# Performance work log

Hardware: AMD Instinct MI355X
Metric: run time of the kernel (lower is better)

## Reference

```python
import jax, jax.numpy as jnp
import numpy as np
import math

B, S, D, H, HD = 2, 2048, 2048, 16, 128
ROPE_THETA = 10000.0


def _rope_cache(seq_len, dim, base, dtype=jnp.float32):
    inv_freq = 1.0 / (base ** (jnp.arange(0, dim, 2, dtype=jnp.float32) / dim))
    t = jnp.arange(seq_len, dtype=jnp.float32)
    freqs = jnp.einsum('i,j->ij', t, inv_freq)          # [S, dim/2]
    emb = jnp.concatenate([freqs, freqs], axis=-1)       # [S, dim]
    return jnp.cos(emb).astype(dtype), jnp.sin(emb).astype(dtype)


def _rotate_half(x):
    x1, x2 = x[..., : x.shape[-1] // 2], x[..., x.shape[-1] // 2:]
    return jnp.concatenate([-x2, x1], axis=-1)


def setup_inputs() -> dict:
    key = jax.random.key(0)
    ks = jax.random.split(key, 6)
    hidden_states = jax.random.normal(ks[0], (B, S, D), dtype=jnp.float32) * 0.02
    w_scale = 1.0 / math.sqrt(D)
    Wq = jax.random.normal(ks[1], (D, D), dtype=jnp.float32) * w_scale
    Wk = jax.random.normal(ks[2], (D, D), dtype=jnp.float32) * w_scale
    Wv = jax.random.normal(ks[3], (D, D), dtype=jnp.float32) * w_scale
    Wo = jax.random.normal(ks[4], (D, D), dtype=jnp.float32) * w_scale
    # additive causal mask [B, 1, S, S]: 0 on/below diag, large negative above
    causal = jnp.tril(jnp.ones((S, S), dtype=bool))
    attention_mask = jnp.where(causal, 0.0, -1e9).astype(jnp.float32)
    attention_mask = jnp.broadcast_to(attention_mask[None, None], (B, 1, S, S))
    position_ids = jnp.broadcast_to(jnp.arange(S, dtype=jnp.int32)[None], (B, S))
    return {
        'hidden_states': hidden_states,
        'attention_mask': attention_mask,
        'position_ids': position_ids,
        'Wq': Wq, 'Wk': Wk, 'Wv': Wv, 'Wo': Wo,
    }


def reference(hidden_states, attention_mask, position_ids, Wq, Wk, Wv, Wo):
    bsz, q_len, _ = hidden_states.shape
    # projections (torch Linear: x @ W.T), then split heads -> [B, H, S, HD]
    def proj(W):
        return jnp.einsum('bsd,ed->bse', hidden_states, W).reshape(bsz, q_len, H, HD).transpose(0, 2, 1, 3)
    q, k, v = proj(Wq), proj(Wk), proj(Wv)
    cos_c, sin_c = _rope_cache(q_len, HD, ROPE_THETA, hidden_states.dtype)
    cos = cos_c[position_ids][:, None]  # [B, 1, S, HD]
    sin = sin_c[position_ids][:, None]
    q = q * cos + _rotate_half(q) * sin
    k = k * cos + _rotate_half(k) * sin
    scores = jnp.einsum('bhqd,bhkd->bhqk', q, k) / math.sqrt(HD)
    scores = scores + attention_mask
    attn_weights = jax.nn.softmax(scores.astype(jnp.float32), axis=-1).astype(q.dtype)
    attn_out = jnp.einsum('bhqk,bhkd->bhqd', attn_weights, v)
    attn_out = attn_out.transpose(0, 2, 1, 3).reshape(bsz, q_len, D)
    out = jnp.einsum('bsd,ed->bse', attn_out, Wo)
    return out
```

## Files before the change

kernel.cpp:

```cpp
#include <hip/hip_runtime.h>

typedef __bf16 bf16;
typedef __bf16 bf16x8 __attribute__((ext_vector_type(8)));
typedef float f32x4 __attribute__((ext_vector_type(4)));

#define D_MODEL 2048
#define SEQ 2048
#define NH 16
#define HEAD_DIM 128
#define NBATCH 2
#define SM_SCALE 0.08838834764831845f
#define WSEG 4194304
#define NT_TILES 32

typedef __attribute__((address_space(1))) const void* gas_cp;
typedef __attribute__((address_space(3))) void* las_p;
__device__ __forceinline__ void ll16(const bf16* g, bf16* l) {
  __builtin_amdgcn_global_load_lds((gas_cp)g, (las_p)l, 16, 0, 0);
}

__device__ __forceinline__ bf16x8 cvt8(const float* p) {
  float4 a = *(const float4*)p;
  float4 b = *(const float4*)(p + 4);
  bf16x8 v;
  v[0] = (bf16)a.x; v[1] = (bf16)a.y; v[2] = (bf16)a.z; v[3] = (bf16)a.w;
  v[4] = (bf16)b.x; v[5] = (bf16)b.y; v[6] = (bf16)b.z; v[7] = (bf16)b.w;
  return v;
}

__global__ __launch_bounds__(256)
void cvt_hidden(const float* __restrict__ src, bf16* __restrict__ dst) {
  size_t i = ((size_t)blockIdx.x * 256 + threadIdx.x) * 8;
  *(bf16x8*)(dst + i) = cvt8(src + i);
}

__global__ __launch_bounds__(256)
void cvt_weights(const float* __restrict__ w0, const float* __restrict__ w1,
                 const float* __restrict__ w2, const float* __restrict__ w3,
                 bf16* __restrict__ dst) {
  const float* src = (blockIdx.y == 0) ? w0 : (blockIdx.y == 1) ? w1
                   : (blockIdx.y == 2) ? w2 : w3;
  size_t i = ((size_t)blockIdx.x * 256 + threadIdx.x) * 8;
  *(bf16x8*)(dst + (size_t)blockIdx.y * WSEG + i) = cvt8(src + i);
}

#define LDFRAG(DA, DB, SB, KX)                                               \
  _Pragma("unroll") for (int mi = 0; mi < 4; mi++)                           \
      DA[mi] = *(const bf16x8*)((SB) + ((arow + mi * 16) << 7) + (KX));      \
  DB[0] = *(const bf16x8*)((SB) + 16384 + (rb0 << 7) + (KX));                \
  DB[1] = *(const bf16x8*)((SB) + 16384 + (rb1 << 7) + (KX));                \
  DB[2] = *(const bf16x8*)((SB) + 16384 + (rb2 << 7) + (KX));                \
  DB[3] = *(const bf16x8*)((SB) + 16384 + (rb3 << 7) + (KX));

#define MMAC(AF, BF)                                                         \
  _Pragma("unroll") for (int mi = 0; mi < 4; mi++)                           \
  _Pragma("unroll") for (int ni = 0; ni < 4; ni++)                           \
      acc[mi][ni] = __builtin_amdgcn_mfma_f32_16x16x32_bf16(                 \
          AF[mi], BF[ni], acc[mi][ni], 0, 0, 0);

#define ST1(GP, ROW0, KT, LB)                                                \
  ll16((GP) + (size_t)((ROW0) + w * 8 + l8) * D_MODEL + (KT) * 64 + kelem,   \
       (bf16*)((LB) + w * 1024));

template <typename TC, int MODE, int NBN>
__global__ __launch_bounds__(512, 2)
void gemm128(const bf16* __restrict__ A, const bf16* __restrict__ W,
             TC* __restrict__ C, bf16* __restrict__ Qo, bf16* __restrict__ Ko,
             bf16* __restrict__ Vo, const int* __restrict__ pos_ids) {
  __shared__ __align__(16) char smem[147456];

  const int tid  = threadIdx.x;
  const int lane = tid & 63;
  const int w    = tid >> 6;
  const int quad = lane >> 4, l15 = lane & 15;
  const int l8   = lane >> 3, l7 = lane & 7;
  const int kelem = 8 * (l7 ^ l8);
  const int wm = w >> 2;
  const int wn = w & 3;
  const int hh = wn >> 1;
  const int cb = (wn & 1) * 32;

  const int nwg = 32 * NBN;
  const int bid = blockIdx.x;
  const int lin = (bid & 7) * (nwg >> 3) + (bid >> 3);
  const int by = lin / NBN, bx = lin % NBN;
  const int mBase = by << 7, nBase = bx << 8;

  const int kx0 = (quad * 16) ^ ((l15 & 7) << 4);
  const int kx1 = kx0 ^ 64;
  const int arow = wm * 64 + l15;
  const int rb0 = hh * 128 + cb + l15;
  const int rb1 = rb0 + 16, rb2 = rb0 + 64, rb3 = rb0 + 80;

  f32x4 acc[4][4];
#pragma unroll
  for (int i = 0; i < 4; i++)
#pragma unroll
    for (int j = 0; j < 4; j++) acc[i][j] = 0.0f;

  bf16x8 aP[4], bP[4];
  bf16x8 aQ[4], bQ[4];

  {
    char* s0 = smem;
    char* s1 = smem + 49152;
    ST1(A, mBase,       0, s0 + 0);
    ST1(A, mBase + 64,  0, s0 + 8192);
    ST1(W, nBase,       0, s0 + 16384);
    ST1(W, nBase + 64,  0, s0 + 24576);
    ST1(W, nBase + 128, 0, s0 + 32768);
    ST1(W, nBase + 192, 0, s0 + 40960);
    ST1(A, mBase,       1, s1 + 0);
    ST1(A, mBase + 64,  1, s1 + 8192);
    ST1(W, nBase,       1, s1 + 16384);
    ST1(W, nBase + 64,  1, s1 + 24576);
    ST1(W, nBase + 128, 1, s1 + 32768);
    ST1(W, nBase + 192, 1, s1 + 40960);
  }
  asm volatile("s_waitcnt vmcnt(6)" ::: "memory");
  __builtin_amdgcn_s_barrier();
  LDFRAG(aP, bP, smem, kx0);

  int buf = 0;
  for (int t = 0; t < NT_TILES; ++t) {
    char* const Sb  = smem + buf * 49152;
    const int  nb1  = (buf + 1 == 3) ? 0 : buf + 1;
    const int  pb   = (buf + 2 >= 3) ? buf - 1 : buf + 2;
    char* const Nb  = smem + nb1 * 49152;
    char* const Pb  = smem + pb * 49152;
    const bool pf   = (t + 2 < NT_TILES);

    LDFRAG(aQ, bQ, Sb, kx1);
    if (pf) {
      ST1(A, mBase,      t + 2, Pb + 0);
      ST1(A, mBase + 64, t + 2, Pb + 8192);
      ST1(W, nBase,      t + 2, Pb + 16384);
    }
    __builtin_amdgcn_sched_barrier(0);
    __builtin_amdgcn_s_setprio(1);
    MMAC(aP, bP);
    __builtin_amdgcn_s_setprio(0);
    asm volatile("s_waitcnt lgkmcnt(0)" ::: "memory");
    if (pf)
      asm volatile("s_waitcnt vmcnt(3)" ::: "memory");
    else
      asm volatile("s_waitcnt vmcnt(0)" ::: "memory");
    __builtin_amdgcn_s_barrier();

    if (t + 1 < NT_TILES) {
      LDFRAG(aP, bP, Nb, kx0);
    }
    if (pf) {
      ST1(W, nBase + 64,  t + 2, Pb + 24576);
      ST1(W, nBase + 128, t + 2, Pb + 32768);
      ST1(W, nBase + 192, t + 2, Pb + 40960);
    }
    __builtin_amdgcn_sched_barrier(0);
    __builtin_amdgcn_s_setprio(1);
    MMAC(aQ, bQ);
    __builtin_amdgcn_s_setprio(0);
    asm volatile("s_waitcnt lgkmcnt(0)" ::: "memory");
    __builtin_amdgcn_s_barrier();

    buf = nb1;
  }

  if (MODE == 0) {
#pragma unroll
    for (int mi = 0; mi < 4; mi++) {
      const int m = mBase + wm * 64 + mi * 16 + quad * 4;
#pragma unroll
      for (int ni = 0; ni < 4; ni++) {
        const int n = nBase + hh * 128 + cb + (ni & 1) * 16 + (ni >> 1) * 64 + l15;
        TC* cp = C + (size_t)m * D_MODEL + n;
#pragma unroll
        for (int r = 0; r < 4; r++) cp[(size_t)r * D_MODEL] = (TC)acc[mi][ni][r];
      }
    }
  } else {
    const int matrix = nBase >> 11;
    const int nb     = nBase & 2047;
    if (matrix == 2) {
      const int h = (nb >> 7) + hh;
#pragma unroll
      for (int mi = 0; mi < 4; mi++)
#pragma unroll
        for (int ni = 0; ni < 4; ni++) {
          const int hd = cb + (ni & 1) * 16 + (ni >> 1) * 64 + l15;
#pragma unroll
          for (int r = 0; r < 4; r++) {
            int m = mBase + wm * 64 + mi * 16 + quad * 4 + r;
            int b = m >> 11, s2 = m & 2047;
            Vo[((size_t)((b * NH + h) * HEAD_DIM + hd)) * SEQ + s2] =
                (bf16)acc[mi][ni][r];
          }
        }
    } else {
      bf16* Out = (matrix == 0) ? Qo : Ko;
      float invf[2];
#pragma unroll
      for (int ni = 0; ni < 2; ni++)
        invf[ni] = __expf(-(float)(cb + ni * 16 + l15) *
                          (9.210340371976184f / 64.0f));
#pragma unroll
      for (int mi = 0; mi < 4; mi++)
#pragma unroll
        for (int r = 0; r < 4; r++) {
          int m = mBase + wm * 64 + mi * 16 + quad * 4 + r;
          float pos = (float)pos_ids[m];
          bf16* op = Out + (size_t)m * D_MODEL + nb + hh * 128 + cb + l15;
#pragma unroll
          for (int ni = 0; ni < 2; ni++) {
            float sn, cs;
            __sincosf(pos * invf[ni], &sn, &cs);
            float q0 = acc[mi][ni][r];
            float q1 = acc[mi][ni + 2][r];
            op[ni * 16]      = (bf16)(q0 * cs - q1 * sn);
            op[ni * 16 + 64] = (bf16)(q1 * cs + q0 * sn);
          }
        }
    }
  }
}

__global__ __launch_bounds__(256, 3)
void attn_mfma(const bf16* __restrict__ Q, const bf16* __restrict__ K,
               const bf16* __restrict__ Vt, bf16* __restrict__ O) {
  __shared__ __align__(16) bf16 K_lds[64 * 136];
  __shared__ __align__(16) bf16 V_lds[128 * 72];
  __shared__ __align__(16) bf16 P_lds[64 * 72];

  const int tid  = threadIdx.x;
  const int lane = tid & 63;
  const int w    = tid >> 6;
  const int quad = lane >> 4, l15 = lane & 15;
  const int s    = 31 - blockIdx.y;
  const int bh   = blockIdx.x;
  const size_t qkBase = (size_t)(bh >> 4) * SEQ * D_MODEL + (size_t)(bh & 15) * HEAD_DIM;
  const size_t vBase  = (size_t)bh * HEAD_DIM * SEQ;

  const int qbase = s * 64 + w * 16;

  bf16x8 qa[4];
#pragma unroll
  for (int kk = 0; kk < 4; kk++)
    qa[kk] = *(const bf16x8*)(Q + qkBase + (size_t)(qbase + l15) * D_MODEL + kk * 32 + quad * 8);

  bf16x8 ones;
#pragma unroll
  for (int i = 0; i < 8; i++) ones[i] = (bf16)1.0f;

  f32x4 oacc[8], ls;
#pragma unroll
  for (int ni = 0; ni < 8; ni++) oacc[ni] = 0.0f;
  ls = 0.0f;

  const int ntiles = s + 1;

  bf16x8 kr[4], vr[4];
  auto loadKV = [&](int t0) {
#pragma unroll
    for (int i = 0; i < 4; i++) {
      int c = tid + 256 * i;
      kr[i] = *(const bf16x8*)(K + qkBase + (size_t)(t0 + (c >> 4)) * D_MODEL + (c & 15) * 8);
    }
#pragma unroll
    for (int i = 0; i < 4; i++) {
      int c = tid + 256 * i;
      vr[i] = *(const bf16x8*)(Vt + vBase + (size_t)(c >> 3) * SEQ + t0 + (c & 7) * 8);
    }
  };
  loadKV(0);

  const int prow = w * 16;

  for (int tt = 0; tt < ntiles; tt++) {
    const int t0 = tt * 64;
    __syncthreads();
#pragma unroll
    for (int i = 0; i < 4; i++) {
      int c = tid + 256 * i;
      *(bf16x8*)&K_lds[(c >> 4) * 136 + (c & 15) * 8] = kr[i];
    }
#pragma unroll
    for (int i = 0; i < 4; i++) {
      int c = tid + 256 * i;
      *(bf16x8*)&V_lds[(c >> 3) * 72 + (c & 7) * 8] = vr[i];
    }
    __syncthreads();
    if (tt + 1 < ntiles) loadKV(t0 + 64);

    f32x4 sacc[4];
#pragma unroll
    for (int ni = 0; ni < 4; ni++) sacc[ni] = 0.0f;
#pragma unroll
    for (int kk = 0; kk < 4; kk++) {
#pragma unroll
      for (int ni = 0; ni < 4; ni++) {
        bf16x8 kf = *(const bf16x8*)&K_lds[(ni * 16 + l15) * 136 + kk * 32 + quad * 8];
        sacc[ni] = __builtin_amdgcn_mfma_f32_16x16x32_bf16(qa[kk], kf, sacc[ni], 0, 0, 0);
      }
    }

    if (tt == s) {
#pragma unroll
      for (int r = 0; r < 4; r++) {
        int qrow = qbase + quad * 4 + r;
#pragma unroll
        for (int ni = 0; ni < 4; ni++) {
          int tcol = t0 + ni * 16 + l15;
          float pv = (tcol <= qrow) ? __expf(fminf(sacc[ni][r] * SM_SCALE, 30.0f)) : 0.0f;
          P_lds[(prow + quad * 4 + r) * 72 + ni * 16 + l15] = (bf16)pv;
        }
      }
    } else {
#pragma unroll
      for (int r = 0; r < 4; r++)
#pragma unroll
        for (int ni = 0; ni < 4; ni++)
          P_lds[(prow + quad * 4 + r) * 72 + ni * 16 + l15] =
              (bf16)__expf(fminf(sacc[ni][r] * SM_SCALE, 30.0f));
    }

#pragma unroll
    for (int kk2 = 0; kk2 < 2; kk2++) {
      bf16x8 pf = *(const bf16x8*)&P_lds[(prow + l15) * 72 + kk2 * 32 + quad * 8];
#pragma unroll
      for (int ni = 0; ni < 8; ni++) {
        bf16x8 vf = *(const bf16x8*)&V_lds[(ni * 16 + l15) * 72 + kk2 * 32 + quad * 8];
        oacc[ni] = __builtin_amdgcn_mfma_f32_16x16x32_bf16(pf, vf, oacc[ni], 0, 0, 0);
      }
      ls = __builtin_amdgcn_mfma_f32_16x16x32_bf16(pf, ones, ls, 0, 0, 0);
    }
  }

#pragma unroll
  for (int r = 0; r < 4; r++) {
    float inv = 1.0f / ls[r];
    bf16* op = O + qkBase + (size_t)(qbase + quad * 4 + r) * D_MODEL;
#pragma unroll
    for (int ni = 0; ni < 8; ni++)
      op[ni * 16 + l15] = (bf16)(oacc[ni][r] * inv);
  }
}

extern "C" void kernel_launch(void* const* d_in, const int* in_sizes, int n_in,
                              void* d_out, int out_size, void* d_ws, size_t ws_size,
                              hipStream_t stream) {
  const float* hidden = (const float*)d_in[0];
  const int* pos = (const int*)d_in[2];
  const float* Wq = (const float*)d_in[3];
  const float* Wk = (const float*)d_in[4];
  const float* Wv = (const float*)d_in[5];
  const float* Wo = (const float*)d_in[6];
  float* out = (float*)d_out;

  const size_t TENS = (size_t)NBATCH * SEQ * D_MODEL;
  bf16* Qb = (bf16*)d_ws;
  bf16* Kb = Qb + TENS;
  bf16* Vt = Kb + TENS;
  bf16* AO = Vt + TENS;
  bf16* Hb = AO + TENS;
  bf16* Wb = Hb + TENS;

  cvt_hidden<<<dim3(TENS / 2048), dim3(256), 0, stream>>>(hidden, Hb);
  cvt_weights<<<dim3(WSEG / 2048, 4), dim3(256), 0, stream>>>(Wq, Wk, Wv, Wo, Wb);

  gemm128<bf16, 1, 24><<<dim3(768), dim3(512), 0, stream>>>(
      Hb, Wb, (bf16*)nullptr, Qb, Kb, Vt, pos);

  attn_mfma<<<dim3(NBATCH * NH, 32), dim3(256), 0, stream>>>(Qb, Kb, Vt, AO);

  gemm128<float, 0, 8><<<dim3(256), dim3(512), 0, stream>>>(
      AO, Wb + 3 * (size_t)WSEG, out, nullptr, nullptr, nullptr, nullptr);
}
```

Measured before the change: 364.6 us.

## Use 256x256 tile GEMM for QKV projection; specialize output projection kernel

Adds a new QKV projection kernel with 256x256 output tiles (8 waves, each computing 128x64). It uses a simpler double-buffered pipeline and keeps the fused RoPE and V-transpose epilogue. This halves the grid to 384 workgroups and raises arithmetic intensity per LDS load, aiming to cut global and LDS traffic per FLOP. The output projection becomes a non-templated kernel with a plainer column mapping. The larger tile doubles accumulator registers, which risks register pressure or spills under launch_bounds(512,2), and the new pipeline waits on vmcnt(0) every tile, giving less overlap.

New measurement: 370.4 us. Within noise of the previous version (+1.6%).

```diff
diff --git a/kernel.cpp b/kernel.cpp
--- a/kernel.cpp
+++ b/kernel.cpp
@@ -44,6 +44,157 @@
   *(bf16x8*)(dst + (size_t)blockIdx.y * WSEG + i) = cvt8(src + i);
 }
 
+#define LDF256(DA, DB, SB, KX)                                               \
+  _Pragma("unroll") for (int mi = 0; mi < 8; mi++)                           \
+      DA[mi] = *(const bf16x8*)((SB) + ((arowQ + mi * 16) << 7) + (KX));     \
+  DB[0] = *(const bf16x8*)((SB) + 32768 + (qb0 << 7) + (KX));                \
+  DB[1] = *(const bf16x8*)((SB) + 32768 + (qb1 << 7) + (KX));                \
+  DB[2] = *(const bf16x8*)((SB) + 32768 + (qb2 << 7) + (KX));                \
+  DB[3] = *(const bf16x8*)((SB) + 32768 + (qb3 << 7) + (KX));
+
+#define MM256(AF, BF)                                                        \
+  _Pragma("unroll") for (int mi = 0; mi < 8; mi++)                           \
+  _Pragma("unroll") for (int ni = 0; ni < 4; ni++)                           \
+      acc[mi][ni] = __builtin_amdgcn_mfma_f32_16x16x32_bf16(                 \
+          AF[mi], BF[ni], acc[mi][ni], 0, 0, 0);
+
+#define ST2(GP, ROW0, KT, LB)                                                \
+  ll16((GP) + (size_t)((ROW0) + w * 8 + l8) * D_MODEL + (KT) * 64 + kelem,   \
+       (bf16*)((LB) + w * 1024));
+
+__global__ __launch_bounds__(512, 2)
+void gemm256(const bf16* __restrict__ A, const bf16* __restrict__ W,
+             bf16* __restrict__ Qo, bf16* __restrict__ Ko,
+             bf16* __restrict__ Vo, const int* __restrict__ pos_ids) {
+  __shared__ __align__(16) char smem[131072];
+
+  const int tid  = threadIdx.x;
+  const int lane = tid & 63;
+  const int w    = tid >> 6;
+  const int quad = lane >> 4, l15 = lane & 15;
+  const int l8   = lane >> 3, l7 = lane & 7;
+  const int kelem = 8 * (l7 ^ l8);
+  const int wm2 = w >> 2;
+  const int wn2 = w & 3;
+  const int hh  = wn2 >> 1;
+  const int cb  = (wn2 & 1) * 32;
+
+  const int bid = blockIdx.x;
+  const int lin = (bid & 7) * 48 + (bid >> 3);
+  const int by = lin / 24, bx = lin % 24;
+  const int mBase = by << 8, nBase = bx << 8;
+
+  const int kx0 = (quad * 16) ^ ((l15 & 7) << 4);
+  const int kx1 = kx0 ^ 64;
+  const int arowQ = wm2 * 128 + l15;
+  const int qb0 = hh * 128 + cb + l15;
+  const int qb1 = qb0 + 16, qb2 = qb0 + 64, qb3 = qb0 + 80;
+
+  f32x4 acc[8][4];
+#pragma unroll
+  for (int i = 0; i < 8; i++)
+#pragma unroll
+    for (int j = 0; j < 4; j++) acc[i][j] = 0.0f;
+
+  bf16x8 aP[8], bP[4];
+  bf16x8 aQ[8], bQ[4];
+
+  {
+    char* s0 = smem;
+    ST2(A, mBase,       0, s0 + 0);
+    ST2(A, mBase + 64,  0, s0 + 8192);
+    ST2(A, mBase + 128, 0, s0 + 16384);
+    ST2(A, mBase + 192, 0, s0 + 24576);
+    ST2(W, nBase,       0, s0 + 32768);
+    ST2(W, nBase + 64,  0, s0 + 40960);
+    ST2(W, nBase + 128, 0, s0 + 49152);
+    ST2(W, nBase + 192, 0, s0 + 57344);
+  }
+  asm volatile("s_waitcnt vmcnt(0)" ::: "memory");
+  __builtin_amdgcn_s_barrier();
+  LDF256(aP, bP, smem, kx0);
+
+  int buf = 0;
+  for (int t = 0; t < NT_TILES; ++t) {
+    char* const Sb = smem + buf * 65536;
+    char* const Ob = smem + (buf ^ 1) * 65536;
+    const bool pf  = (t + 1 < NT_TILES);
+
+    LDF256(aQ, bQ, Sb, kx1);
+    if (pf) {
+      ST2(A, mBase,       t + 1, Ob + 0);
+      ST2(A, mBase + 64,  t + 1, Ob + 8192);
+      ST2(A, mBase + 128, t + 1, Ob + 16384);
+      ST2(A, mBase + 192, t + 1, Ob + 24576);
+      ST2(W, nBase,       t + 1, Ob + 32768);
+      ST2(W, nBase + 64,  t + 1, Ob + 40960);
+      ST2(W, nBase + 128, t + 1, Ob + 49152);
+      ST2(W, nBase + 192, t + 1, Ob + 57344);
+    }
+    __builtin_amdgcn_sched_barrier(0);
+    __builtin_amdgcn_s_setprio(1);
+    MM256(aP, bP);
+    __builtin_amdgcn_s_setprio(0);
+    asm volatile("s_waitcnt lgkmcnt(0)" ::: "memory");
+    asm volatile("s_waitcnt vmcnt(0)" ::: "memory");
+    __builtin_amdgcn_s_barrier();
+
+    if (pf) {
+      LDF256(aP, bP, Ob, kx0);
+    }
+    __builtin_amdgcn_sched_barrier(0);
+    __builtin_amdgcn_s_setprio(1);
+    MM256(aQ, bQ);
+    __builtin_amdgcn_s_setprio(0);
+    asm volatile("s_waitcnt lgkmcnt(0)" ::: "memory");
+
+    buf ^= 1;
+  }
+
+  const int matrix = nBase >> 11;
+  const int nb     = nBase & 2047;
+  if (matrix == 2) {
+    const int h = (nb >> 7) + hh;
+#pragma unroll
+    for (int mi = 0; mi < 8; mi++)
+#pragma unroll
+      for (int ni = 0; ni < 4; ni++) {
+        const int hd = cb + (ni & 1) * 16 + (ni >> 1) * 64 + l15;
+#pragma unroll
+        for (int r = 0; r < 4; r++) {
+          int m = mBase + wm2 * 128 + mi * 16 + quad * 4 + r;
+          int b = m >> 11, s2 = m & 2047;
+          Vo[((size_t)((b * NH + h) * HEAD_DIM + hd)) * SEQ + s2] =
+              (bf16)acc[mi][ni][r];
+        }
+      }
+  } else {
+    bf16* Out = (matrix == 0) ? Qo : Ko;
+    float invf[2];
+#pragma unroll
+    for (int ni = 0; ni < 2; ni++)
+      invf[ni] = __expf(-(float)(cb + ni * 16 + l15) *
+                        (9.210340371976184f / 64.0f));
+#pragma unroll
+    for (int mi = 0; mi < 8; mi++)
+#pragma unroll
+      for (int r = 0; r < 4; r++) {
+        int m = mBase + wm2 * 128 + mi * 16 + quad * 4 + r;
+        float pos = (float)pos_ids[m];
+        bf16* op = Out + (size_t)m * D_MODEL + nb + hh * 128 + cb + l15;
+#pragma unroll
+        for (int ni = 0; ni < 2; ni++) {
+          float sn, cs;
+          __sincosf(pos * invf[ni], &sn, &cs);
+          float q0 = acc[mi][ni][r];
+          float q1 = acc[mi][ni + 2][r];
+          op[ni * 16]      = (bf16)(q0 * cs - q1 * sn);
+          op[ni * 16 + 64] = (bf16)(q1 * cs + q0 * sn);
+        }
+      }
+  }
+}
+
 #define LDFRAG(DA, DB, SB, KX)                                               \
   _Pragma("unroll") for (int mi = 0; mi < 4; mi++)                           \
       DA[mi] = *(const bf16x8*)((SB) + ((arow + mi * 16) << 7) + (KX));      \
@@ -62,11 +213,9 @@
   ll16((GP) + (size_t)((ROW0) + w * 8 + l8) * D_MODEL + (KT) * 64 + kelem,   \
        (bf16*)((LB) + w * 1024));
 
-template <typename TC, int MODE, int NBN>
 __global__ __launch_bounds__(512, 2)
-void gemm128(const bf16* __restrict__ A, const bf16* __restrict__ W,
-             TC* __restrict__ C, bf16* __restrict__ Qo, bf16* __restrict__ Ko,
-             bf16* __restrict__ Vo, const int* __restrict__ pos_ids) {
+void gemm_proj(const bf16* __restrict__ A, const bf16* __restrict__ W,
+               float* __restrict__ C) {
   __shared__ __align__(16) char smem[147456];
 
   const int tid  = threadIdx.x;
@@ -77,20 +226,17 @@
   const int kelem = 8 * (l7 ^ l8);
   const int wm = w >> 2;
   const int wn = w & 3;
-  const int hh = wn >> 1;
-  const int cb = (wn & 1) * 32;
-
-  const int nwg = 32 * NBN;
+
   const int bid = blockIdx.x;
-  const int lin = (bid & 7) * (nwg >> 3) + (bid >> 3);
-  const int by = lin / NBN, bx = lin % NBN;
+  const int lin = (bid & 7) * 32 + (bid >> 3);
+  const int by = lin >> 3, bx = lin & 7;
   const int mBase = by << 7, nBase = bx << 8;
 
   const int kx0 = (quad * 16) ^ ((l15 & 7) << 4);
   const int kx1 = kx0 ^ 64;
   const int arow = wm * 64 + l15;
-  const int rb0 = hh * 128 + cb + l15;
-  const int rb1 = rb0 + 16, rb2 = rb0 + 64, rb3 = rb0 + 80;
+  const int rb0 = wn * 64 + l15;
+  const int rb1 = rb0 + 16, rb2 = rb0 + 32, rb3 = rb0 + 48;
 
   f32x4 acc[4][4];
 #pragma unroll
@@ -98,8 +244,7 @@
 #pragma unroll
     for (int j = 0; j < 4; j++) acc[i][j] = 0.0f;
 
-  bf16x8 aP[4], bP[4];
-  bf16x8 aQ[4], bQ[4];
+  bf16x8 aP[4], bP[4], aQ[4], bQ[4];
 
   {
     char* s0 = smem;
@@ -165,60 +310,15 @@
     buf = nb1;
   }
 
-  if (MODE == 0) {
-#pragma unroll
-    for (int mi = 0; mi < 4; mi++) {
-      const int m = mBase + wm * 64 + mi * 16 + quad * 4;
-#pragma unroll
-      for (int ni = 0; ni < 4; ni++) {
-        const int n = nBase + hh * 128 + cb + (ni & 1) * 16 + (ni >> 1) * 64 + l15;
-        TC* cp = C + (size_t)m * D_MODEL + n;
-#pragma unroll
-        for (int r = 0; r < 4; r++) cp[(size_t)r * D_MODEL] = (TC)acc[mi][ni][r];
-      }
-    }
-  } else {
-    const int matrix = nBase >> 11;
-    const int nb     = nBase & 2047;
-    if (matrix == 2) {
-      const int h = (nb >> 7) + hh;
-#pragma unroll
-      for (int mi = 0; mi < 4; mi++)
-#pragma unroll
-        for (int ni = 0; ni < 4; ni++) {
-          const int hd = cb + (ni & 1) * 16 + (ni >> 1) * 64 + l15;
-#pragma unroll
-          for (int r = 0; r < 4; r++) {
-            int m = mBase + wm * 64 + mi * 16 + quad * 4 + r;
-            int b = m >> 11, s2 = m & 2047;
-            Vo[((size_t)((b * NH + h) * HEAD_DIM + hd)) * SEQ + s2] =
-                (bf16)acc[mi][ni][r];
-          }
-        }
-    } else {
-      bf16* Out = (matrix == 0) ? Qo : Ko;
-      float invf[2];
-#pragma unroll
-      for (int ni = 0; ni < 2; ni++)
-        invf[ni] = __expf(-(float)(cb + ni * 16 + l15) *
-                          (9.210340371976184f / 64.0f));
-#pragma unroll
-      for (int mi = 0; mi < 4; mi++)
-#pragma unroll
-        for (int r = 0; r < 4; r++) {
-          int m = mBase + wm * 64 + mi * 16 + quad * 4 + r;
-          float pos = (float)pos_ids[m];
-          bf16* op = Out + (size_t)m * D_MODEL + nb + hh * 128 + cb + l15;
-#pragma unroll
-          for (int ni = 0; ni < 2; ni++) {
-            float sn, cs;
-            __sincosf(pos * invf[ni], &sn, &cs);
-            float q0 = acc[mi][ni][r];
-            float q1 = acc[mi][ni + 2][r];
-            op[ni * 16]      = (bf16)(q0 * cs - q1 * sn);
-            op[ni * 16 + 64] = (bf16)(q1 * cs + q0 * sn);
-          }
-        }
+#pragma unroll
+  for (int mi = 0; mi < 4; mi++) {
+    const int m = mBase + wm * 64 + mi * 16 + quad * 4;
+#pragma unroll
+    for (int ni = 0; ni < 4; ni++) {
+      const int n = nBase + wn * 64 + ni * 16 + l15;
+      float* cp = C + (size_t)m * D_MODEL + n;
+#pragma unroll
+      for (int r = 0; r < 4; r++) cp[(size_t)r * D_MODEL] = acc[mi][ni][r];
     }
   }
 }
@@ -366,11 +466,10 @@
   cvt_hidden<<<dim3(TENS / 2048), dim3(256), 0, stream>>>(hidden, Hb);
   cvt_weights<<<dim3(WSEG / 2048, 4), dim3(256), 0, stream>>>(Wq, Wk, Wv, Wo, Wb);
 
-  gemm128<bf16, 1, 24><<<dim3(768), dim3(512), 0, stream>>>(
-      Hb, Wb, (bf16*)nullptr, Qb, Kb, Vt, pos);
+  gemm256<<<dim3(384), dim3(512), 0, stream>>>(Hb, Wb, Qb, Kb, Vt, pos);
 
   attn_mfma<<<dim3(NBATCH * NH, 32), dim3(256), 0, stream>>>(Qb, Kb, Vt, AO);
 
-  gemm128<float, 0, 8><<<dim3(256), dim3(512), 0, stream>>>(
-      AO, Wb + 3 * (size_t)WSEG, out, nullptr, nullptr, nullptr, nullptr);
-}
+  gemm_proj<<<dim3(256), dim3(512), 0, stream>>>(
+      AO, Wb + 3 * (size_t)WSEG, out);
+}
```
